# Performance work log

Measured on AMD Instinct MI355X. Metric: run time of the kernel, lower is better.

The kernel has to match this reference:

```python
import jax, jax.numpy as jnp
import numpy as np

CLAMP_MIN = 0.001
DOWN = 4  # ROI module downsampling factor


def setup_inputs() -> dict:
    key = jax.random.key(0)
    ks = jax.random.split(key, 12)
    B, I, H, W = 2, 63, 320, 320
    C, HID, CTX = 14, 128, 192
    h4, w4 = H // DOWN, W // DOWN
    return {
        "depth": jnp.zeros((B, 1, H, W), jnp.float32),
        "context": jax.random.normal(ks[0], (B, CTX, h4, w4), jnp.float32),
        "input_feature_map": jax.random.normal(ks[1], (B, HID, h4, w4), jnp.float32),
        "bin_num": 16,
        "min_depth": 1,
        "max_depth": 10,
        "masks": jnp.zeros((B, 1, H, W), jnp.float32),
        "instances": jax.random.randint(ks[2], (B, I, H, W), 0, 2).astype(jnp.int32),
        "boxes": jax.random.randint(ks[3], (B, I, 4), 0, W).astype(jnp.int32),
        "labels": jax.random.randint(ks[4], (B, I), 0, C).astype(jnp.int32),
        # per-class scale/shift heads (row 0 = invalid class, gathered but masked out)
        "W_scale": (jax.random.normal(ks[5], (C, HID), jnp.float32) * 0.05),
        "b_scale": (jax.random.normal(ks[6], (C,), jnp.float32) * 0.05),
        "W_shift": (jax.random.normal(ks[7], (C, HID), jnp.float32) * 0.05),
        "b_shift": (jax.random.normal(ks[8], (C,), jnp.float32) * 0.05),
        # shared canonical head: 1x1 conv 128 -> 1
        "Wc": (jax.random.normal(ks[9], (HID,), jnp.float32) * 0.05),
        "bc": (jax.random.normal(ks[10], (), jnp.float32) * 0.05),
    }


def reference(depth, context, input_feature_map, bin_num, min_depth, max_depth,
              masks, instances, boxes, labels,
              W_scale, b_scale, W_shift, b_shift, Wc, bc):
    B, I, H, W = instances.shape
    m = instances.astype(input_feature_map.dtype)            # [B,I,H,W] binary instance masks
    m_ds = m[:, :, ::DOWN, ::DOWN]                            # [B,I,H/4,W/4] mask at feature res
    valid = (labels != 0).astype(input_feature_map.dtype)     # [B,I]

    # Per-instance mask-pooled feature (vectorized gather over all instances/classes)
    denom = jnp.maximum(m_ds.sum(axis=(-1, -2)), 1.0)         # [B,I]
    pooled = jnp.einsum('bihw,bchw->bic', m_ds, input_feature_map) / denom[..., None]  # [B,I,HID]

    # Per-class scale/shift heads, gathered by label; zero where label==0
    scale = (jnp.einsum('bic,bic->bi', pooled, W_scale[labels]) + b_scale[labels]) * valid  # [B,I]
    shift = (jnp.einsum('bic,bic->bi', pooled, W_shift[labels]) + b_shift[labels]) * valid  # [B,I]

    # invalid instances stay zero (mirrors zero-init scatter of canonical_full)
    can_small = jnp.einsum('bchw,c->bhw', input_feature_map, Wc) + bc   # [B,H/4,W/4]
    can = jnp.repeat(jnp.repeat(can_small, DOWN, axis=-2), DOWN, axis=-1)  # [B,H,W]
    canonical_full = can[:, None] * m * valid[..., None, None]          # [B,I,H,W]

    # loss_type == 0 path: relu then clamp(min=0.001)
    depth_instances_r = jnp.maximum(
        jax.nn.relu(canonical_full * scale[..., None, None] + shift[..., None, None]),
        CLAMP_MIN)

    return depth_instances_r, canonical_full, scale, shift
```

## Files before the change

kernel.cpp:

```cpp
#include <hip/hip_runtime.h>

#define NB 2
#define NI 63
#define BI (NB*NI)
#define HW 320
#define HWF (HW*HW)
#define H4 80
#define HW4 (H4*H4)
#define HID 128
#define IFM_B (HID*HW4)

#define OUT_DEPTH 0
#define OUT_CAN   (BI*HWF)
#define OUT_SCALE (2*BI*HWF)
#define OUT_SHIFT (2*BI*HWF + BI)

#define KB 128
#define NKB (HW4/KB)
#define FPAD 132
#define PROW 132
#define PBLK (64*PROW)

__global__ __launch_bounds__(256) void pool_gemm_kernel(
    const int* __restrict__ inst, const float* __restrict__ ifm,
    const float* __restrict__ Wc, const float* __restrict__ bc,
    float* __restrict__ can_ws, float* __restrict__ partial) {
  __shared__ float fT[128][FPAD];
  __shared__ float mT[64][FPAD];
  __shared__ float wc_s[128];

  int bid = blockIdx.x;
  int b = bid / NKB, kb = bid % NKB;
  int k0 = kb * KB;
  int t = threadIdx.x;

  if (t < 128) wc_s[t] = Wc[t];

  const float* fbase = ifm + (long)b * IFM_B;
#pragma unroll
  for (int s = 0; s < 16; ++s) {
    int v = s * 256 + t;
    int c = v >> 5;
    int jq = v & 31;
    float4 x = *(const float4*)(fbase + c * HW4 + k0 + jq * 4);
    *(float4*)&fT[c][jq * 4] = x;
  }
#pragma unroll
  for (int s = 0; s < 32; ++s) {
    int v = s * 256 + t;
    int i = v >> 7;
    int j = v & 127;
    int hw4 = k0 + j;
    int r = hw4 / H4, col = hw4 - r * H4;
    float m = 0.f;
    if (i < NI) m = (float)inst[((long)(b * NI + i)) * HWF + r * 4 * HW + col * 4];
    mT[i][j] = m;
  }
  __syncthreads();

  int ti = t >> 4, tc = t & 15;
  int i0 = ti * 4;
  float acc[4][8];
#pragma unroll
  for (int u = 0; u < 4; ++u)
#pragma unroll
    for (int v = 0; v < 8; ++v) acc[u][v] = 0.f;

  for (int k = 0; k < KB; k += 4) {
    float4 a[4], bb[8];
#pragma unroll
    for (int u = 0; u < 4; ++u) a[u] = *(const float4*)&mT[i0 + u][k];
#pragma unroll
    for (int v = 0; v < 8; ++v) bb[v] = *(const float4*)&fT[tc + 16 * v][k];
#pragma unroll
    for (int u = 0; u < 4; ++u)
#pragma unroll
      for (int v = 0; v < 8; ++v)
        acc[u][v] += a[u].x * bb[v].x + a[u].y * bb[v].y +
                     a[u].z * bb[v].z + a[u].w * bb[v].w;
  }

  float* pb = partial + (long)bid * PBLK;
#pragma unroll
  for (int u = 0; u < 4; ++u)
#pragma unroll
    for (int v = 0; v < 8; ++v)
      pb[(i0 + u) * PROW + tc + 16 * v] = acc[u][v];

  if (t < 64) {
    float ms = 0.f;
#pragma unroll
    for (int q = 0; q < KB / 4; ++q) {
      float4 m4 = *(const float4*)&mT[t][q * 4];
      ms += m4.x + m4.y + m4.z + m4.w;
    }
    pb[t * PROW + 128] = ms;
  }

  if (t < 128) {
    float ca = bc[0];
#pragma unroll 8
    for (int c = 0; c < 128; ++c) ca += fT[c][t] * wc_s[c];
    can_ws[b * HW4 + k0 + t] = ca;
  }
}

__global__ __launch_bounds__(128) void finish_kernel(
    const float* __restrict__ partial, const int* __restrict__ labels,
    const float* __restrict__ W_scale, const float* __restrict__ b_scale,
    const float* __restrict__ W_shift, const float* __restrict__ b_shift,
    float* __restrict__ scale_out, float* __restrict__ shift_out) {
  __shared__ float pooled[128];
  __shared__ float msum_s;

  int bi = blockIdx.x;
  int b = bi / NI, i = bi % NI;
  int t = threadIdx.x;
  int lane = t & 63;

  const float* pb = partial + ((long)b * NKB) * PBLK + i * PROW;

  float acc = 0.f;
#pragma unroll 5
  for (int kb = 0; kb < NKB; ++kb) acc += pb[(long)kb * PBLK + t];
  pooled[t] = acc;

  if (t < 64) {
    float ms = (t < NKB) ? pb[(long)t * PBLK + 128] : 0.f;
    for (int off = 32; off; off >>= 1) ms += __shfl_down(ms, off, 64);
    if (t == 0) msum_s = ms;
  }
  __syncthreads();

  if (t < 64) {
    int lab = labels[bi];
    float valid = (lab != 0) ? 1.f : 0.f;
    float inv = 1.f / fmaxf(msum_s, 1.f);
    float p0 = pooled[lane], p1 = pooled[lane + 64];
    const float* ws = W_scale + lab * HID;
    const float* wh = W_shift + lab * HID;
    float sa = p0 * ws[lane] + p1 * ws[lane + 64];
    float sh = p0 * wh[lane] + p1 * wh[lane + 64];
    for (int off = 32; off; off >>= 1) {
      sa += __shfl_down(sa, off, 64);
      sh += __shfl_down(sh, off, 64);
    }
    if (lane == 0) {
      scale_out[bi] = (sa * inv + b_scale[lab]) * valid;
      shift_out[bi] = (sh * inv + b_shift[lab]) * valid;
    }
  }
}

__global__ __launch_bounds__(256) void out_kernel(
    const int* __restrict__ inst, const float* __restrict__ can_ws,
    const int* __restrict__ labels,
    const float* __restrict__ scale_arr, const float* __restrict__ shift_arr,
    float* __restrict__ out_depth, float* __restrict__ out_can) {
  int blk = blockIdx.x;
  int bi = blk / 100;
  int chunk = blk - bi * 100;
  int b = bi / NI;
  int pix = chunk * 1024 + threadIdx.x * 4;
  int h = pix / HW, w = pix - h * HW;

  float can = can_ws[b * HW4 + (h >> 2) * H4 + (w >> 2)];
  int lab = labels[bi];
  float valid = (lab != 0) ? 1.f : 0.f;
  float sc = scale_arr[bi];
  float sh = shift_arr[bi];
  float cv = can * valid;

  long base = (long)bi * HWF + pix;
  const int4 iv = *(const int4*)(inst + base);
  float4 cf, df;
  cf.x = cv * (float)iv.x;
  cf.y = cv * (float)iv.y;
  cf.z = cv * (float)iv.z;
  cf.w = cv * (float)iv.w;
  df.x = fmaxf(cf.x * sc + sh, 0.001f);
  df.y = fmaxf(cf.y * sc + sh, 0.001f);
  df.z = fmaxf(cf.z * sc + sh, 0.001f);
  df.w = fmaxf(cf.w * sc + sh, 0.001f);
  *(float4*)(out_can + base) = cf;
  *(float4*)(out_depth + base) = df;
}

extern "C" void kernel_launch(void* const* d_in, const int* in_sizes, int n_in,
                              void* d_out, int out_size, void* d_ws, size_t ws_size,
                              hipStream_t stream) {
  const float* ifm     = (const float*)d_in[2];
  const int*   inst    = (const int*)d_in[7];
  const int*   labels  = (const int*)d_in[9];
  const float* W_scale = (const float*)d_in[10];
  const float* b_scale = (const float*)d_in[11];
  const float* W_shift = (const float*)d_in[12];
  const float* b_shift = (const float*)d_in[13];
  const float* Wc      = (const float*)d_in[14];
  const float* bc      = (const float*)d_in[15];

  float* out       = (float*)d_out;
  float* out_depth = out + OUT_DEPTH;
  float* out_can   = out + OUT_CAN;
  float* out_scale = out + OUT_SCALE;
  float* out_shift = out + OUT_SHIFT;

  float* can_ws  = (float*)d_ws;
  float* partial = (float*)d_ws + 2 * HW4;

  pool_gemm_kernel<<<NB * NKB, 256, 0, stream>>>(inst, ifm, Wc, bc,
                                                 can_ws, partial);
  finish_kernel<<<BI, 128, 0, stream>>>(partial, labels, W_scale, b_scale,
                                        W_shift, b_shift, out_scale, out_shift);
  out_kernel<<<BI * 100, 256, 0, stream>>>(inst, can_ws, labels, out_scale,
                                           out_shift, out_depth, out_can);
}
```

Before: 205.8 us.

## Halve pool GEMM K-tile, widen blocks, use nontemporal streaming in output kernel

The pooling GEMM tile along the spatial dimension is halved and the block widened to 512 threads. This doubles the block count to spread the strided mask gathers and the GEMM over more CUs, at the cost of twice as many partial rows for the finish kernel to reduce. The output kernel now handles 8 pixels per thread and uses nontemporal loads and stores for the large instance read and the two output writes, to avoid polluting cache on pure streaming traffic. The mask gathers in the GEMM also use nontemporal loads.

```diff
diff --git a/kernel.cpp b/kernel.cpp
--- a/kernel.cpp
+++ b/kernel.cpp
@@ -15,13 +15,16 @@
 #define OUT_SCALE (2*BI*HWF)
 #define OUT_SHIFT (2*BI*HWF + BI)
 
-#define KB 128
+#define KB 64
 #define NKB (HW4/KB)
-#define FPAD 132
+#define FPAD 68
 #define PROW 132
 #define PBLK (64*PROW)
 
-__global__ __launch_bounds__(256) void pool_gemm_kernel(
+typedef int   vint4  __attribute__((ext_vector_type(4)));
+typedef float vflt4  __attribute__((ext_vector_type(4)));
+
+__global__ __launch_bounds__(512) void pool_gemm_kernel(
     const int* __restrict__ inst, const float* __restrict__ ifm,
     const float* __restrict__ Wc, const float* __restrict__ bc,
     float* __restrict__ can_ws, float* __restrict__ partial) {
@@ -38,44 +41,46 @@
 
   const float* fbase = ifm + (long)b * IFM_B;
 #pragma unroll
-  for (int s = 0; s < 16; ++s) {
-    int v = s * 256 + t;
-    int c = v >> 5;
-    int jq = v & 31;
+  for (int s = 0; s < 4; ++s) {
+    int v = s * 512 + t;
+    int c = v >> 4;
+    int jq = v & 15;
     float4 x = *(const float4*)(fbase + c * HW4 + k0 + jq * 4);
     *(float4*)&fT[c][jq * 4] = x;
   }
 #pragma unroll
-  for (int s = 0; s < 32; ++s) {
-    int v = s * 256 + t;
-    int i = v >> 7;
-    int j = v & 127;
+  for (int s = 0; s < 8; ++s) {
+    int v = s * 512 + t;
+    int i = v >> 6;
+    int j = v & 63;
     int hw4 = k0 + j;
     int r = hw4 / H4, col = hw4 - r * H4;
     float m = 0.f;
-    if (i < NI) m = (float)inst[((long)(b * NI + i)) * HWF + r * 4 * HW + col * 4];
+    if (i < NI)
+      m = (float)__builtin_nontemporal_load(
+          inst + ((long)(b * NI + i)) * HWF + r * 4 * HW + col * 4);
     mT[i][j] = m;
   }
   __syncthreads();
 
-  int ti = t >> 4, tc = t & 15;
+  int ti = t >> 5, tc = t & 31;
   int i0 = ti * 4;
-  float acc[4][8];
+  float acc[4][4];
 #pragma unroll
   for (int u = 0; u < 4; ++u)
 #pragma unroll
-    for (int v = 0; v < 8; ++v) acc[u][v] = 0.f;
+    for (int v = 0; v < 4; ++v) acc[u][v] = 0.f;
 
   for (int k = 0; k < KB; k += 4) {
-    float4 a[4], bb[8];
+    float4 a[4], bb[4];
 #pragma unroll
     for (int u = 0; u < 4; ++u) a[u] = *(const float4*)&mT[i0 + u][k];
 #pragma unroll
-    for (int v = 0; v < 8; ++v) bb[v] = *(const float4*)&fT[tc + 16 * v][k];
+    for (int v = 0; v < 4; ++v) bb[v] = *(const float4*)&fT[tc + 32 * v][k];
 #pragma unroll
     for (int u = 0; u < 4; ++u)
 #pragma unroll
-      for (int v = 0; v < 8; ++v)
+      for (int v = 0; v < 4; ++v)
         acc[u][v] += a[u].x * bb[v].x + a[u].y * bb[v].y +
                      a[u].z * bb[v].z + a[u].w * bb[v].w;
   }
@@ -84,8 +89,8 @@
 #pragma unroll
   for (int u = 0; u < 4; ++u)
 #pragma unroll
-    for (int v = 0; v < 8; ++v)
-      pb[(i0 + u) * PROW + tc + 16 * v] = acc[u][v];
+    for (int v = 0; v < 4; ++v)
+      pb[(i0 + u) * PROW + tc + 32 * v] = acc[u][v];
 
   if (t < 64) {
     float ms = 0.f;
@@ -95,9 +100,7 @@
       ms += m4.x + m4.y + m4.z + m4.w;
     }
     pb[t * PROW + 128] = ms;
-  }
-
-  if (t < 128) {
+
     float ca = bc[0];
 #pragma unroll 8
     for (int c = 0; c < 128; ++c) ca += fT[c][t] * wc_s[c];
@@ -121,12 +124,13 @@
   const float* pb = partial + ((long)b * NKB) * PBLK + i * PROW;
 
   float acc = 0.f;
-#pragma unroll 5
+#pragma unroll 4
   for (int kb = 0; kb < NKB; ++kb) acc += pb[(long)kb * PBLK + t];
   pooled[t] = acc;
 
   if (t < 64) {
-    float ms = (t < NKB) ? pb[(long)t * PBLK + 128] : 0.f;
+    float ms = pb[(long)t * PBLK + 128];
+    if (t + 64 < NKB) ms += pb[(long)(t + 64) * PBLK + 128];
     for (int off = 32; off; off >>= 1) ms += __shfl_down(ms, off, 64);
     if (t == 0) msum_s = ms;
   }
@@ -158,32 +162,44 @@
     const float* __restrict__ scale_arr, const float* __restrict__ shift_arr,
     float* __restrict__ out_depth, float* __restrict__ out_can) {
   int blk = blockIdx.x;
-  int bi = blk / 100;
-  int chunk = blk - bi * 100;
+  int bi = blk / 50;
+  int chunk = blk - bi * 50;
   int b = bi / NI;
-  int pix = chunk * 1024 + threadIdx.x * 4;
+  int pix = chunk * 2048 + threadIdx.x * 8;
   int h = pix / HW, w = pix - h * HW;
 
-  float can = can_ws[b * HW4 + (h >> 2) * H4 + (w >> 2)];
+  const float2 c2 = *(const float2*)(can_ws + b * HW4 + (h >> 2) * H4 + (w >> 2));
   int lab = labels[bi];
   float valid = (lab != 0) ? 1.f : 0.f;
   float sc = scale_arr[bi];
   float sh = shift_arr[bi];
-  float cv = can * valid;
+  float cv0 = c2.x * valid;
+  float cv1 = c2.y * valid;
 
   long base = (long)bi * HWF + pix;
-  const int4 iv = *(const int4*)(inst + base);
-  float4 cf, df;
-  cf.x = cv * (float)iv.x;
-  cf.y = cv * (float)iv.y;
-  cf.z = cv * (float)iv.z;
-  cf.w = cv * (float)iv.w;
-  df.x = fmaxf(cf.x * sc + sh, 0.001f);
-  df.y = fmaxf(cf.y * sc + sh, 0.001f);
-  df.z = fmaxf(cf.z * sc + sh, 0.001f);
-  df.w = fmaxf(cf.w * sc + sh, 0.001f);
-  *(float4*)(out_can + base) = cf;
-  *(float4*)(out_depth + base) = df;
+  const vint4 iv0 = __builtin_nontemporal_load((const vint4*)(inst + base));
+  const vint4 iv1 = __builtin_nontemporal_load((const vint4*)(inst + base + 4));
+  vflt4 cf0, cf1, df0, df1;
+  cf0.x = cv0 * (float)iv0.x;
+  cf0.y = cv0 * (float)iv0.y;
+  cf0.z = cv0 * (float)iv0.z;
+  cf0.w = cv0 * (float)iv0.w;
+  cf1.x = cv1 * (float)iv1.x;
+  cf1.y = cv1 * (float)iv1.y;
+  cf1.z = cv1 * (float)iv1.z;
+  cf1.w = cv1 * (float)iv1.w;
+  df0.x = fmaxf(cf0.x * sc + sh, 0.001f);
+  df0.y = fmaxf(cf0.y * sc + sh, 0.001f);
+  df0.z = fmaxf(cf0.z * sc + sh, 0.001f);
+  df0.w = fmaxf(cf0.w * sc + sh, 0.001f);
+  df1.x = fmaxf(cf1.x * sc + sh, 0.001f);
+  df1.y = fmaxf(cf1.y * sc + sh, 0.001f);
+  df1.z = fmaxf(cf1.z * sc + sh, 0.001f);
+  df1.w = fmaxf(cf1.w * sc + sh, 0.001f);
+  __builtin_nontemporal_store(cf0, (vflt4*)(out_can + base));
+  __builtin_nontemporal_store(cf1, (vflt4*)(out_can + base + 4));
+  __builtin_nontemporal_store(df0, (vflt4*)(out_depth + base));
+  __builtin_nontemporal_store(df1, (vflt4*)(out_depth + base + 4));
 }
 
 extern "C" void kernel_launch(void* const* d_in, const int* in_sizes, int n_in,
@@ -208,10 +224,10 @@
   float* can_ws  = (float*)d_ws;
   float* partial = (float*)d_ws + 2 * HW4;
 
-  pool_gemm_kernel<<<NB * NKB, 256, 0, stream>>>(inst, ifm, Wc, bc,
+  pool_gemm_kernel<<<NB * NKB, 512, 0, stream>>>(inst, ifm, Wc, bc,
                                                  can_ws, partial);
   finish_kernel<<<BI, 128, 0, stream>>>(partial, labels, W_scale, b_scale,
                                         W_shift, b_shift, out_scale, out_shift);
-  out_kernel<<<BI * 100, 256, 0, stream>>>(inst, can_ws, labels, out_scale,
-                                           out_shift, out_depth, out_can);
-}
+  out_kernel<<<BI * 50, 256, 0, stream>>>(inst, can_ws, labels, out_scale,
+                                          out_shift, out_depth, out_can);
+}
```

Result: no change. 206.8 us (+0.5%).
